# Kernel optimization log

Measured on AMD Instinct MI355X. Metric: run time of the kernel, lower is better.

Reference implementation:

```python
import jax, jax.numpy as jnp
import numpy as np

B, D_IN, R, D_P, K, D_C, ITERS = 4096, 2048, 7, 128, 25, 16, 3


def _ln(x, g, b, eps=1e-5):
    m = jnp.mean(x, axis=-1, keepdims=True)
    v = jnp.var(x, axis=-1, keepdims=True)
    return (x - m) * jax.lax.rsqrt(v + eps) * g + b


def _squash(x):
    eps = 1e-6
    ns = jnp.sum(x * x, axis=-1, keepdims=True)
    scale = ns / jnp.maximum(1.0 + ns, eps)
    return scale * x / (jnp.sqrt(ns) + eps)


def setup_inputs() -> dict:
    key = jax.random.key(0)
    ks = jax.random.split(key, 8)
    f = lambda k, shp, s=0.02: (jax.random.normal(k, shp) * s).astype(jnp.float32)
    return {
        "z": jax.random.normal(ks[0], (B, D_IN), jnp.float32),
        "W_prim": f(ks[1], (D_IN, R * D_P)),
        "b_prim": jnp.zeros((R * D_P,), jnp.float32),
        "ln_a_g": jnp.ones((D_IN,), jnp.float32),
        "ln_a_b": jnp.zeros((D_IN,), jnp.float32),
        "W_act": f(ks[2], (D_IN, R)),
        "b_act": jnp.zeros((R,), jnp.float32),
        "w_caps": (np.sqrt(K / (D_P * R)).astype(np.float32)
                   * jax.random.normal(ks[3], (R, D_P, K, D_C))).astype(jnp.float32),
        "ln_c_g": jnp.ones((D_C,), jnp.float32),
        "ln_c_b": jnp.zeros((D_C,), jnp.float32),
        "beta_u": f(ks[4], (K,), 1.0),
        "ln_h_g": jnp.ones((R * D_C,), jnp.float32),
        "ln_h_b": jnp.zeros((R * D_C,), jnp.float32),
        "W_h1": f(ks[5], (R * D_C, 4 * R * D_C)),
        "b_h1": jnp.zeros((4 * R * D_C,), jnp.float32),
        "W_h2": f(ks[6], (4 * R * D_C, 1)),
        "b_h2": jnp.zeros((1,), jnp.float32),
    }


def reference(z, W_prim, b_prim, ln_a_g, ln_a_b, W_act, b_act, w_caps,
              ln_c_g, ln_c_b, beta_u, ln_h_g, ln_h_b, W_h1, b_h1, W_h2, b_h2):
    # primary capsules: [B, R, D_P] poses + [B, R] activations
    pose = _squash((z @ W_prim + b_prim).reshape(B, R, D_P))
    act = jnp.clip(jax.nn.sigmoid(_ln(z, ln_a_g, ln_a_b) @ W_act + b_act), 0.0, 1.0)

    # votes: [B, R, K, D_C]
    u = jnp.einsum('brd,rdkh->brkh', pose, w_caps)
    scale = 1.0 / np.sqrt(D_C).astype(np.float32)

    # iterative routing (EM/softmax-agreement style)
    q = jnp.full((B, R, K), 1.0 / K, dtype=z.dtype)
    class_pose = None
    for _ in range(ITERS):
        wts = q * act[:, :, None]                               # [B,R,K]
        class_pose = _ln(jnp.einsum('brk,brkh->bkh', wts, u), ln_c_g, ln_c_b)
        agree = jnp.einsum('bkh,brkh->brk', class_pose, u) * scale
        q = jax.nn.softmax(agree, axis=-1)

    class_act = jax.nn.sigmoid(beta_u[None, :] + jnp.einsum('brk,br->bk', q, act))
    route_class_emb = q[..., None] * u                          # [B,R,K,D_C]

    # concat per-route interaction vectors -> [B, K, R*D_C]
    class_embed = jnp.transpose(route_class_emb, (0, 2, 1, 3)).reshape(B, K, R * D_C)
    h = jax.nn.gelu(_ln(class_embed, ln_h_g, ln_h_b) @ W_h1 + b_h1, approximate=False)
    logits = (h @ W_h2 + b_h2)[..., 0]                          # [B, K]

    return (logits, class_embed, class_pose, class_act, q, pose, act, route_class_emb)
```

## Files before the change

### kernel.cpp

```cpp
#include <hip/hip_runtime.h>
#include <cstddef>

#define BB 4096
#define DIN 2048
#define RR 7
#define DP 128
#define KK 25
#define DC 16
#define NITERS 3
#define RKH (RR*KK*DC)
#define RK  (RR*KK)
#define KH  (KK*DC)
#define HD  (RR*DC)
#define H4  (4*HD)
#define HEAD_TILES (BB*KK/128)

typedef __attribute__((ext_vector_type(8))) short bf16x8;
typedef __attribute__((ext_vector_type(4))) float f32x4;

__device__ __forceinline__ unsigned pk_bf16(float a, float b) {
    union { float f; unsigned u; } xa, xb;
    xa.f = a; xb.f = b;
    unsigned ua = (xa.u + 0x7FFFu + ((xa.u >> 16) & 1u)) >> 16;
    unsigned ub = (xb.u + 0x7FFFu + ((xb.u >> 16) & 1u)) >> 16;
    return (ua & 0xFFFFu) | (ub << 16);
}

__device__ __forceinline__ unsigned short bf16_1(float a) {
    union { float f; unsigned u; } xa; xa.f = a;
    return (unsigned short)((xa.u + 0x7FFFu + ((xa.u >> 16) & 1u)) >> 16);
}

__device__ __forceinline__ float gelu_fast(float x) {
    float u = x * __builtin_fmaf(x * x, 0.07135655f, 1.5957691f);
    u = fmaxf(u, -30.0f);
    float e = __expf(-u);
    return x * __builtin_amdgcn_rcpf(1.0f + e);
}

__global__ __launch_bounds__(256) void transpose_cvt_kernel(
    const float* __restrict__ src, unsigned short* __restrict__ dst, int RS, int CS)
{
    __shared__ float T[64][65];
    int r0 = blockIdx.x * 64, c0 = blockIdx.y * 64;
    size_t bo = (size_t)blockIdx.z * RS * CS;
    src += bo; dst += bo;
    int t = threadIdx.x;
    for (int s = t; s < 64 * 16; s += 256) {
        int row = s >> 4, c4 = s & 15;
        int gr = r0 + row, gc = c0 + c4 * 4;
        float4 v = make_float4(0.f, 0.f, 0.f, 0.f);
        if (gr < RS && gc < CS) v = *(const float4*)(src + (size_t)gr * CS + gc);
        T[row][c4 * 4 + 0] = v.x; T[row][c4 * 4 + 1] = v.y;
        T[row][c4 * 4 + 2] = v.z; T[row][c4 * 4 + 3] = v.w;
    }
    __syncthreads();
    for (int s = t; s < 64 * 16; s += 256) {
        int col = s >> 4, r4 = s & 15;
        int gc = c0 + col, gr = r0 + r4 * 4;
        if (gc < CS && gr + 3 < RS) {
            unsigned lo = pk_bf16(T[r4 * 4 + 0][col], T[r4 * 4 + 1][col]);
            unsigned hi = pk_bf16(T[r4 * 4 + 2][col], T[r4 * 4 + 3][col]);
            *(uint2*)(dst + (size_t)gc * RS + gr) = make_uint2(lo, hi);
        }
    }
}

__global__ __launch_bounds__(256) void w1_frag_kernel(
    const float* __restrict__ W1, unsigned short* __restrict__ W1F)
{
    int d = blockIdx.x * 256 + threadIdx.x;
    int e2 = d & 3;
    int lane = (d >> 2) & 63;
    int fid = d >> 8;
    int j = fid & 3, ks = (fid >> 2) & 3, nc = fid >> 4;
    int col = nc * 64 + j * 16 + (lane & 15);
    int k = ks * 32 + (lane >> 4) * 8 + e2 * 2;
    float a = (k < HD)     ? W1[(size_t)k * H4 + col]       : 0.f;
    float b = (k + 1 < HD) ? W1[(size_t)(k + 1) * H4 + col] : 0.f;
    ((unsigned*)W1F)[d] = pk_bf16(a, b);
}

__global__ __launch_bounds__(256) void wpf_kernel(
    const float* __restrict__ Wp, unsigned short* __restrict__ wpf)
{
    int tid = blockIdx.x * 256 + threadIdx.x;
    int lane = tid & 63;
    int CH = tid >> 6;
    int c = CH & 63, gcol = CH >> 6;
    int n = gcol * 16 + (lane & 15);
    int k0 = c * 32 + (lane >> 4) * 8;
    unsigned d0, d1, d2, d3;
    {
        float a0 = Wp[(size_t)(k0 + 0) * (RR * DP) + n];
        float a1 = Wp[(size_t)(k0 + 1) * (RR * DP) + n];
        float a2 = Wp[(size_t)(k0 + 2) * (RR * DP) + n];
        float a3 = Wp[(size_t)(k0 + 3) * (RR * DP) + n];
        float a4 = Wp[(size_t)(k0 + 4) * (RR * DP) + n];
        float a5 = Wp[(size_t)(k0 + 5) * (RR * DP) + n];
        float a6 = Wp[(size_t)(k0 + 6) * (RR * DP) + n];
        float a7 = Wp[(size_t)(k0 + 7) * (RR * DP) + n];
        d0 = pk_bf16(a0, a1); d1 = pk_bf16(a2, a3);
        d2 = pk_bf16(a4, a5); d3 = pk_bf16(a6, a7);
    }
    *(uint4*)(wpf + (size_t)tid * 8) = make_uint4(d0, d1, d2, d3);
}

__global__ __launch_bounds__(256) void wcf_kernel(
    const float* __restrict__ wc, unsigned short* __restrict__ wcf)
{
    __shared__ float Sw[128][17];
    int r = blockIdx.x, nt = blockIdx.y;
    int t = threadIdx.x;
    {
        int d = t >> 1, half = t & 1;
        const float* sp = wc + ((size_t)r * DP + d) * KH + nt * 16 + half * 8;
        float4 v0 = *(const float4*)(sp);
        float4 v1 = *(const float4*)(sp + 4);
        Sw[d][half * 8 + 0] = v0.x; Sw[d][half * 8 + 1] = v0.y;
        Sw[d][half * 8 + 2] = v0.z; Sw[d][half * 8 + 3] = v0.w;
        Sw[d][half * 8 + 4] = v1.x; Sw[d][half * 8 + 5] = v1.y;
        Sw[d][half * 8 + 6] = v1.z; Sw[d][half * 8 + 7] = v1.w;
    }
    __syncthreads();
    int l = t >> 2, e2 = t & 3;
    int n = l & 15;
    unsigned* outp = (unsigned*)wcf;
#pragma unroll
    for (int c = 0; c < 4; ++c) {
        int d = c * 32 + (l >> 4) * 8 + e2 * 2;
        unsigned v = pk_bf16(Sw[d][n], Sw[d + 1][n]);
        outp[(size_t)((r * 100 + nt * 4 + c)) * 256 + t] = v;
    }
}

__global__ __launch_bounds__(256) void act_kernel(
    const float* __restrict__ z, const float* __restrict__ g, const float* __restrict__ bb,
    const float* __restrict__ Wa, const float* __restrict__ ba,
    float* __restrict__ act_out, unsigned short* __restrict__ zf_out)
{
    int b = blockIdx.x;
    int t = threadIdx.x;
    __shared__ float zs[DIN];
    __shared__ float ws1[4], ws2[4];
    __shared__ float wr[4][RR];
    const float* zr = z + (size_t)b * DIN;
    float s = 0.f, s2 = 0.f;
    for (int i = t; i < DIN; i += 256) {
        float v = zr[i]; zs[i] = v; s += v; s2 += v * v;
    }
    for (int off = 32; off; off >>= 1) { s += __shfl_down(s, off); s2 += __shfl_down(s2, off); }
    int w = t >> 6, lane = t & 63;
    if (lane == 0) { ws1[w] = s; ws2[w] = s2; }
    __syncthreads();
    if (zf_out) {
        int c = t >> 2, o = t & 3;
        const float* zp = zs + c * 32 + o * 8;
        unsigned d0 = pk_bf16(zp[0], zp[1]);
        unsigned d1 = pk_bf16(zp[2], zp[3]);
        unsigned d2 = pk_bf16(zp[4], zp[5]);
        unsigned d3 = pk_bf16(zp[6], zp[7]);
        size_t off2 = (((size_t)(b >> 4) * 64 + c) * 64 + (size_t)(o * 16 + (b & 15))) * 8;
        *(uint4*)(zf_out + off2) = make_uint4(d0, d1, d2, d3);
    }
    s  = ws1[0] + ws1[1] + ws1[2] + ws1[3];
    s2 = ws2[0] + ws2[1] + ws2[2] + ws2[3];
    float mean = s * (1.0f / DIN);
    float var  = s2 * (1.0f / DIN) - mean * mean;
    float rstd = rsqrtf(var + 1e-5f);
    float acc[RR];
#pragma unroll
    for (int r = 0; r < RR; ++r) acc[r] = 0.f;
    for (int i = t; i < DIN; i += 256) {
        float y = (zs[i] - mean) * rstd * g[i] + bb[i];
#pragma unroll
        for (int r = 0; r < RR; ++r) acc[r] += y * Wa[i * RR + r];
    }
    for (int off = 32; off; off >>= 1) {
#pragma unroll
        for (int r = 0; r < RR; ++r) acc[r] += __shfl_down(acc[r], off);
    }
    if (lane == 0) {
#pragma unroll
        for (int r = 0; r < RR; ++r) wr[w][r] = acc[r];
    }
    __syncthreads();
    if (t < RR) {
        float v = wr[0][t] + wr[1][t] + wr[2][t] + wr[3][t] + ba[t];
        float sg = 1.0f / (1.0f + expf(-v));
        sg = fminf(fmaxf(sg, 0.0f), 1.0f);
        act_out[(size_t)b * RR + t] = sg;
    }
}

#define PV_STAGE(KS, AD, BD) do {                                                           \
    _Pragma("unroll")                                                                       \
    for (int q = 0; q < 4; ++q) {                                                           \
        int ch = w * 4 + q;                                                                 \
        int gi = ch >> 2, cc = ch & 3;                                                      \
        __builtin_amdgcn_global_load_lds(                                                   \
            (const __attribute__((address_space(1))) unsigned int*)(const void*)            \
                (zf + (((size_t)(zbase + gi) * 64) + (KS) * 4 + cc) * 512 + l * 8),         \
            (__attribute__((address_space(3))) unsigned int*)(void*)                        \
                ((AD) + ch * 512 + l * 8), 16, 0, 0);                                       \
        __builtin_amdgcn_global_load_lds(                                                   \
            (const __attribute__((address_space(1))) unsigned int*)(const void*)            \
                (wpf + (((size_t)(wbase + gi) * 64) + (KS) * 4 + cc) * 512 + l * 8),        \
            (__attribute__((address_space(3))) unsigned int*)(void*)                        \
                ((BD) + ch * 512 + l * 8), 16, 0, 0);                                       \
    }                                                                                       \
} while (0)

#define PV_COMPUTE(AD, BD) do {                                                             \
    _Pragma("unroll")                                                                       \
    for (int c = 0; c < 4; ++c) {                                                           \
        bf16x8 a[2], b[4];                                                                  \
        _Pragma("unroll")                                                                   \
        for (int i = 0; i < 2; ++i)                                                         \
            a[i] = *(const bf16x8*)((AD) + ((wrI * 2 + i) * 4 + c) * 512 + l * 8);          \
        _Pragma("unroll")                                                                   \
        for (int j = 0; j < 4; ++j)                                                         \
            b[j] = *(const bf16x8*)((BD) + ((wcI * 4 + j) * 4 + c) * 512 + l * 8);          \
        _Pragma("unroll")                                                                   \
        for (int i = 0; i < 2; ++i)                                                         \
            _Pragma("unroll")                                                               \
            for (int j = 0; j < 4; ++j)                                                     \
                acc[i][j] = __builtin_amdgcn_mfma_f32_16x16x32_bf16(a[i], b[j], acc[i][j], 0, 0, 0); \
    }                                                                                       \
} while (0)

__global__ __launch_bounds__(512) void pose_votes_mfma(
    const unsigned short* __restrict__ zf, const unsigned short* __restrict__ wpf,
    const unsigned short* __restrict__ wcf, const float* __restrict__ bp,
    float* __restrict__ pose_out, float* __restrict__ u_out)
{
    __shared__ __align__(16) char pool[135168];
    __shared__ float sq[2][128];
    unsigned short* A0 = (unsigned short*)pool;
    unsigned short* A1 = (unsigned short*)(pool + 32768);
    unsigned short* B0 = (unsigned short*)(pool + 65536);
    unsigned short* B1 = (unsigned short*)(pool + 98304);
    unsigned short* AT = (unsigned short*)pool;
    unsigned short* BV = (unsigned short*)(pool + 32768);

    int m0 = blockIdx.x * 128, r = blockIdx.y;
    int t = threadIdx.x, w = t >> 6, l = t & 63;
    int wrI = w >> 1, wcI = w & 1;
    int lrow = l & 15, koff = l >> 4;
    int zbase = m0 >> 4;
    int wbase = r * 8;

    f32x4 acc[2][4];
#pragma unroll
    for (int i = 0; i < 2; ++i)
#pragma unroll
        for (int j = 0; j < 4; ++j) acc[i][j] = 0.0f;

    PV_STAGE(0, A0, B0);
    __syncthreads();
#pragma unroll 1
    for (int ks = 0; ks < 16; ks += 2) {
        if (ks + 1 < 16) PV_STAGE(ks + 1, A1, B1);
        PV_COMPUTE(A0, B0);
        __syncthreads();
        if (ks + 2 < 16) PV_STAGE(ks + 2, A0, B0);
        PV_COMPUTE(A1, B1);
        __syncthreads();
    }

    const unsigned short* wrp = wcf + (size_t)r * 100 * 512;
#pragma unroll
    for (int q = 0; q < 13; ++q) {
        int chunk = w + q * 8;
        if (chunk < 100)
            __builtin_amdgcn_global_load_lds(
                (const __attribute__((address_space(1))) unsigned int*)(const void*)(wrp + (size_t)chunk * 512 + l * 8),
                (__attribute__((address_space(3))) unsigned int*)(void*)(BV + chunk * 512),
                16, 0, 0);
    }

    float bpv[4];
#pragma unroll
    for (int j = 0; j < 4; ++j) bpv[j] = bp[r * DP + wcI * 64 + j * 16 + lrow];
    float ns_[2][4];
#pragma unroll
    for (int i = 0; i < 2; ++i)
#pragma unroll
        for (int reg = 0; reg < 4; ++reg) {
            float ss = 0.f;
#pragma unroll
            for (int j = 0; j < 4; ++j) {
                float x = acc[i][j][reg] + bpv[j];
                acc[i][j][reg] = x;
                ss += x * x;
            }
            ss += __shfl_xor(ss, 1); ss += __shfl_xor(ss, 2);
            ss += __shfl_xor(ss, 4); ss += __shfl_xor(ss, 8);
            ns_[i][reg] = ss;
        }
    if (lrow == 0) {
#pragma unroll
        for (int i = 0; i < 2; ++i)
#pragma unroll
            for (int reg = 0; reg < 4; ++reg)
                sq[wcI][wrI * 32 + i * 16 + koff * 4 + reg] = ns_[i][reg];
    }
    __syncthreads();

#pragma unroll
    for (int i = 0; i < 2; ++i)
#pragma unroll
        for (int reg = 0; reg < 4; ++reg) {
            int rl = wrI * 32 + i * 16 + koff * 4 + reg;
            float ns = sq[0][rl] + sq[1][rl];
            float factor = (ns / fmaxf(1.0f + ns, 1e-6f)) / (sqrtf(ns) + 1e-6f);
            size_t rowbase = ((size_t)(m0 + rl) * RR + r) * DP;
            int g8 = rl >> 4, r15 = rl & 15;
#pragma unroll
            for (int j = 0; j < 4; ++j) {
                float v = acc[i][j][reg] * factor;
                int col = wcI * 64 + j * 16 + lrow;
                pose_out[rowbase + col] = v;
                int cseg = col >> 5;
                int l2 = r15 + 16 * ((col >> 3) & 3);
                AT[(size_t)((g8 * 4 + cseg) * 64 + l2) * 8 + (col & 7)] = bf16_1(v);
            }
        }
    __syncthreads();

    bf16x8 af2[4];
#pragma unroll
    for (int c = 0; c < 4; ++c)
        af2[c] = *(const bf16x8*)(AT + (size_t)((w * 4 + c) * 64 + l) * 8);
    int crow = (l >> 4) * 4;
#pragma unroll 1
    for (int nt = 0; nt < 25; ++nt) {
        f32x4 a2 = 0.0f;
#pragma unroll
        for (int c = 0; c < 4; ++c) {
            bf16x8 bfr = *(const bf16x8*)(BV + (size_t)((nt * 4 + c) * 64 + l) * 8);
            a2 = __builtin_amdgcn_mfma_f32_16x16x32_bf16(af2[c], bfr, a2, 0, 0, 0);
        }
#pragma unroll
        for (int reg = 0; reg < 4; ++reg) {
            int row = m0 + w * 16 + crow + reg;
            u_out[((size_t)row * RR + r) * KH + nt * 16 + (l & 15)] = a2[reg];
        }
    }
}

__global__ __launch_bounds__(256) void pose_mfma(
    const float* __restrict__ z, const unsigned short* __restrict__ WpT,
    const float* __restrict__ bp, float* __restrict__ pose_out)
{
    __shared__ __align__(16) unsigned short As[128 * 40];
    __shared__ __align__(16) unsigned short Bs[128 * 40];
    __shared__ float sq[2][128];
    int m0 = blockIdx.x * 128, r = blockIdx.y, t = threadIdx.x;
    int n0 = r * DP;
    int w = t >> 6, l = t & 63;
    int lrow = l & 15, koff = l >> 4;
    int rbase = (w >> 1) * 64, cbase = (w & 1) * 64;
    f32x4 acc[4][4];
#pragma unroll
    for (int i = 0; i < 4; ++i)
#pragma unroll
        for (int j = 0; j < 4; ++j) acc[i][j] = 0.0f;
    for (int kt = 0; kt < DIN; kt += 32) {
#pragma unroll
        for (int q = 0; q < 4; ++q) {
            int s = t + 256 * q;
            int row = s >> 3, k4 = s & 7;
            float4 v = *(const float4*)(z + (size_t)(m0 + row) * DIN + kt + k4 * 4);
            *(uint2*)(As + row * 40 + k4 * 4) = make_uint2(pk_bf16(v.x, v.y), pk_bf16(v.z, v.w));
        }
#pragma unroll
        for (int q = 0; q < 2; ++q) {
            int s = t + 256 * q;
            int col = s >> 2, k8 = s & 3;
            uint4 v = *(const uint4*)(WpT + (size_t)(n0 + col) * DIN + kt + k8 * 8);
            *(uint4*)(Bs + col * 40 + k8 * 8) = v;
        }
        __syncthreads();
        bf16x8 a[4], b[4];
#pragma unroll
        for (int i = 0; i < 4; ++i)
            a[i] = *(const bf16x8*)(As + (rbase + i * 16 + lrow) * 40 + koff * 8);
#pragma unroll
        for (int j = 0; j < 4; ++j)
            b[j] = *(const bf16x8*)(Bs + (cbase + j * 16 + lrow) * 40 + koff * 8);
#pragma unroll
        for (int i = 0; i < 4; ++i)
#pragma unroll
            for (int j = 0; j < 4; ++j)
                acc[i][j] = __builtin_amdgcn_mfma_f32_16x16x32_bf16(a[i], b[j], acc[i][j], 0, 0, 0);
        __syncthreads();
    }
    float bpv[4];
#pragma unroll
    for (int j = 0; j < 4; ++j) bpv[j] = bp[n0 + cbase + j * 16 + lrow];
    float ns_[4][4];
#pragma unroll
    for (int i = 0; i < 4; ++i)
#pragma unroll
        for (int reg = 0; reg < 4; ++reg) {
            float ss = 0.f;
#pragma unroll
            for (int j = 0; j < 4; ++j) {
                float x = acc[i][j][reg] + bpv[j];
                acc[i][j][reg] = x;
                ss += x * x;
            }
            ss += __shfl_xor(ss, 1); ss += __shfl_xor(ss, 2);
            ss += __shfl_xor(ss, 4); ss += __shfl_xor(ss, 8);
            ns_[i][reg] = ss;
        }
    if (lrow == 0) {
#pragma unroll
        for (int i = 0; i < 4; ++i)
#pragma unroll
            for (int reg = 0; reg < 4; ++reg)
                sq[w & 1][rbase + i * 16 + koff * 4 + reg] = ns_[i][reg];
    }
    __syncthreads();
#pragma unroll
    for (int i = 0; i < 4; ++i)
#pragma unroll
        for (int reg = 0; reg < 4; ++reg) {
            int rl = rbase + i * 16 + koff * 4 + reg;
            float ns = sq[0][rl] + sq[1][rl];
            float factor = (ns / fmaxf(1.0f + ns, 1e-6f)) / (sqrtf(ns) + 1e-6f);
            size_t rowbase = ((size_t)(m0 + rl) * RR + r) * DP;
#pragma unroll
            for (int j = 0; j < 4; ++j)
                pose_out[rowbase + cbase + j * 16 + lrow] = acc[i][j][reg] * factor;
        }
}

__global__ __launch_bounds__(256) void votes_mfma(
    const float* __restrict__ pose, const unsigned short* __restrict__ wcT,
    float* __restrict__ u_out)
{
    __shared__ __align__(16) unsigned short As[128 * 152];
    __shared__ __align__(16) unsigned short Bs[80 * 152];
    int m0 = blockIdx.x * 128, r = blockIdx.y, n0 = blockIdx.z * 80;
    int t = threadIdx.x;
    int w = t >> 6, l = t & 63;
    int lrow = l & 15, koff = l >> 4;
    int rbase = w * 32;
#pragma unroll
    for (int q = 0; q < 16; ++q) {
        int s = t + 256 * q;
        int row = s >> 5, k4 = s & 31;
        float4 v = *(const float4*)(pose + ((size_t)(m0 + row) * RR + r) * DP + k4 * 4);
        *(uint2*)(As + row * 152 + k4 * 4) = make_uint2(pk_bf16(v.x, v.y), pk_bf16(v.z, v.w));
    }
    const unsigned short* wr_ = wcT + (size_t)r * KH * DP;
#pragma unroll
    for (int q = 0; q < 5; ++q) {
        int s = t + 256 * q;
        int col = s >> 4, k8 = s & 15;
        uint4 v = *(const uint4*)(wr_ + (size_t)(n0 + col) * DP + k8 * 8);
        *(uint4*)(Bs + col * 152 + k8 * 8) = v;
    }
    __syncthreads();
    f32x4 acc[2][5];
#pragma unroll
    for (int i = 0; i < 2; ++i)
#pragma unroll
        for (int j = 0; j < 5; ++j) acc[i][j] = 0.0f;
#pragma unroll
    for (int ks = 0; ks < 4; ++ks) {
        bf16x8 a[2], b[5];
#pragma unroll
        for (int i = 0; i < 2; ++i)
            a[i] = *(const bf16x8*)(As + (rbase + i * 16 + lrow) * 152 + ks * 32 + koff * 8);
#pragma unroll
        for (int j = 0; j < 5; ++j)
            b[j] = *(const bf16x8*)(Bs + (j * 16 + lrow) * 152 + ks * 32 + koff * 8);
#pragma unroll
        for (int i = 0; i < 2; ++i)
#pragma unroll
            for (int j = 0; j < 5; ++j)
                acc[i][j] = __builtin_amdgcn_mfma_f32_16x16x32_bf16(a[i], b[j], acc[i][j], 0, 0, 0);
    }
#pragma unroll
    for (int i = 0; i < 2; ++i)
#pragma unroll
        for (int reg = 0; reg < 4; ++reg) {
            int row = m0 + rbase + i * 16 + koff * 4 + reg;
            size_t base = ((size_t)row * RR + r) * KH + n0;
#pragma unroll
            for (int j = 0; j < 5; ++j)
                u_out[base + j * 16 + lrow] = acc[i][j][reg];
        }
}

__global__ __launch_bounds__(64) void routing_kernel(
    const float* __restrict__ u_in, const float* __restrict__ act_in,
    const float* __restrict__ lncg, const float* __restrict__ lncb,
    const float* __restrict__ beta_u,
    float* __restrict__ q_out, float* __restrict__ cp_out,
    float* __restrict__ ca_out, float* __restrict__ rce_out,
    float* __restrict__ ce_out)
{
    __shared__ __align__(16) float U[RKH];
    __shared__ float Q[RK];
    __shared__ float CP[KH];
    __shared__ float AG[RK];
    __shared__ float A7[RR];
    int b = blockIdx.x, t = threadIdx.x;
    const float4* u4 = (const float4*)(u_in + (size_t)b * RKH);
    float4* U4 = (float4*)U;
    for (int p = t; p < RKH / 4; p += 64) U4[p] = u4[p];
    if (t < RR) A7[t] = act_in[(size_t)b * RR + t];
    for (int p = t; p < RK; p += 64) Q[p] = 1.0f / KK;
    __syncthreads();
    for (int it = 0; it < NITERS; ++it) {
        for (int p = t; p < KH; p += 64) {
            int k = p / DC;
            float s = 0.f;
#pragma unroll
            for (int r = 0; r < RR; ++r) s += Q[r * KK + k] * A7[r] * U[r * KH + p];
            CP[p] = s;
        }
        __syncthreads();
        if (t < KK) {
            float m = 0.f;
#pragma unroll
            for (int h = 0; h < DC; ++h) m += CP[t * DC + h];
            m *= (1.0f / DC);
            float v = 0.f;
#pragma unroll
            for (int h = 0; h < DC; ++h) { float d = CP[t * DC + h] - m; v += d * d; }
            v *= (1.0f / DC);
            float rstd = rsqrtf(v + 1e-5f);
#pragma unroll
            for (int h = 0; h < DC; ++h)
                CP[t * DC + h] = (CP[t * DC + h] - m) * rstd * lncg[h] + lncb[h];
        }
        __syncthreads();
        for (int p = t; p < RK; p += 64) {
            int r = p / KK, k = p % KK;
            float s = 0.f;
#pragma unroll
            for (int h = 0; h < DC; ++h) s += CP[k * DC + h] * U[r * KH + k * DC + h];
            AG[p] = s * 0.25f;
        }
        __syncthreads();
        if (t < RR) {
            float mx = -1e30f;
            for (int k = 0; k < KK; ++k) mx = fmaxf(mx, AG[t * KK + k]);
            float e[KK], sum = 0.f;
            for (int k = 0; k < KK; ++k) { e[k] = expf(AG[t * KK + k] - mx); sum += e[k]; }
            float inv = 1.0f / sum;
            for (int k = 0; k < KK; ++k) Q[t * KK + k] = e[k] * inv;
        }
        __syncthreads();
    }
    if (t < KK) {
        float s = 0.f;
#pragma unroll
        for (int r = 0; r < RR; ++r) s += Q[r * KK + t] * A7[r];
        ca_out[(size_t)b * KK + t] = 1.0f / (1.0f + expf(-(beta_u[t] + s)));
    }
    for (int p = t; p < RK; p += 64) q_out[(size_t)b * RK + p] = Q[p];
    for (int p = t; p < KH; p += 64) cp_out[(size_t)b * KH + p] = CP[p];
    float4* rce4 = (float4*)(rce_out + (size_t)b * RKH);
    float4* ce4  = (float4*)ce_out;
    for (int p4 = t; p4 < RKH / 4; p4 += 64) {
        int base = p4 * 4;
        int r  = base / KH;
        int k  = (base % KH) / DC;
        int h0 = base % DC;
        float qv = Q[r * KK + k];
        float4 uv = U4[p4];
        float4 rv = make_float4(qv * uv.x, qv * uv.y, qv * uv.z, qv * uv.w);
        rce4[p4] = rv;
        size_t ci = ((size_t)b * RKH + (size_t)k * HD + (size_t)r * DC + h0) >> 2;
        ce4[ci] = rv;
    }
}

__global__ __launch_bounds__(512) void head_mfma(
    const float* __restrict__ ce, const float* __restrict__ g, const float* __restrict__ bb,
    const unsigned short* __restrict__ W1F, const float* __restrict__ b1,
    const float* __restrict__ W2, const float* __restrict__ b2,
    float* __restrict__ logits)
{
    __shared__ __align__(16) unsigned short As[128 * 128];
    __shared__ __align__(16) unsigned short Bs[448 * 128];
    __shared__ float LB1[H4];
    __shared__ float LW2[H4];
    int t = threadIdx.x;
    int w = t >> 6, l = t & 63;
    int lrow = l & 15, koff = l >> 4;

#pragma unroll
    for (int q = 0; q < 14; ++q) {
        int chunk = w * 14 + q;
        __builtin_amdgcn_global_load_lds(
            (const __attribute__((address_space(1))) unsigned int*)(const void*)(W1F + (size_t)chunk * 512 + l * 8),
            (__attribute__((address_space(3))) unsigned int*)(void*)(Bs + chunk * 512),
            16, 0, 0);
    }
    if (t >= 256) {
        for (int s = t - 256; s < H4; s += 256) { LB1[s] = b1[s]; LW2[s] = W2[s]; }
    }
    float b2v = b2[0];

    int row = t >> 1, half = t & 1;
    int lr = row & 15, rt = row >> 4;

    float4 v[14];
    int tile = blockIdx.x;
    if (t < 256 && tile < HEAD_TILES) {
        const float* rp = ce + (size_t)(tile * 128 + row) * HD + half * 56;
#pragma unroll
        for (int m = 0; m < 14; ++m) v[m] = *(const float4*)(rp + m * 4);
    }

    bool first = true;
    for (; tile < HEAD_TILES; tile += 256) {
        if (!first) __syncthreads();
        first = false;

        if (t < 256) {
            float s1 = 0.f, s2 = 0.f;
#pragma unroll
            for (int m = 0; m < 14; ++m) {
                s1 += v[m].x + v[m].y + v[m].z + v[m].w;
                s2 += v[m].x * v[m].x + v[m].y * v[m].y + v[m].z * v[m].z + v[m].w * v[m].w;
            }
            s1 += __shfl_xor(s1, 1); s2 += __shfl_xor(s2, 1);
            float mean = s1 * (1.0f / HD);
            float var  = s2 * (1.0f / HD) - mean * mean;
            float rstd = rsqrtf(var + 1e-5f);
#pragma unroll
            for (int j = 0; j < 7; ++j) {
                float4 gl0 = *(const float4*)(g  + half * 56 + j * 8);
                float4 gl1 = *(const float4*)(g  + half * 56 + j * 8 + 4);
                float4 bl0 = *(const float4*)(bb + half * 56 + j * 8);
                float4 bl1 = *(const float4*)(bb + half * 56 + j * 8 + 4);
                float4 x0 = v[j * 2], x1 = v[j * 2 + 1];
                float y0 = (x0.x - mean) * rstd * gl0.x + bl0.x;
                float y1 = (x0.y - mean) * rstd * gl0.y + bl0.y;
                float y2 = (x0.z - mean) * rstd * gl0.z + bl0.z;
                float y3 = (x0.w - mean) * rstd * gl0.w + bl0.w;
                float y4 = (x1.x - mean) * rstd * gl1.x + bl1.x;
                float y5 = (x1.y - mean) * rstd * gl1.y + bl1.y;
                float y6 = (x1.z - mean) * rstd * gl1.z + bl1.z;
                float y7 = (x1.w - mean) * rstd * gl1.w + bl1.w;
                int k8 = half * 7 + j;
                int ks = k8 >> 2, ko = k8 & 3;
                unsigned* dst = (unsigned*)(As + (size_t)((rt * 4 + ks) * 64 + ko * 16 + lr) * 8);
                dst[0] = pk_bf16(y0, y1); dst[1] = pk_bf16(y2, y3);
                dst[2] = pk_bf16(y4, y5); dst[3] = pk_bf16(y6, y7);
            }
            if (half) {
                uint4 z4 = make_uint4(0, 0, 0, 0);
                *(uint4*)(As + (size_t)((rt * 4 + 3) * 64 + 2 * 16 + lr) * 8) = z4;
                *(uint4*)(As + (size_t)((rt * 4 + 3) * 64 + 3 * 16 + lr) * 8) = z4;
            }
        }
        __syncthreads();

        bf16x8 af[4];
#pragma unroll
        for (int ks = 0; ks < 4; ++ks)
            af[ks] = *(const bf16x8*)(As + (size_t)((w * 4 + ks) * 64 + l) * 8);

        if (t < 256 && tile + 256 < HEAD_TILES) {
            const float* rp = ce + (size_t)((tile + 256) * 128 + row) * HD + half * 56;
#pragma unroll
            for (int m = 0; m < 14; ++m) v[m] = *(const float4*)(rp + m * 4);
        }

        float logitAcc[4];
#pragma unroll
        for (int reg = 0; reg < 4; ++reg) logitAcc[reg] = 0.f;

        for (int nc = 0; nc < 7; ++nc) {
            float b1v[4], w2v[4];
#pragma unroll
            for (int j = 0; j < 4; ++j) {
                b1v[j] = LB1[nc * 64 + j * 16 + lrow];
                w2v[j] = LW2[nc * 64 + j * 16 + lrow];
            }
            f32x4 acc[4];
#pragma unroll
            for (int j = 0; j < 4; ++j) acc[j] = 0.0f;
#pragma unroll
            for (int ks = 0; ks < 4; ++ks) {
                bf16x8 bfr[4];
#pragma unroll
                for (int j = 0; j < 4; ++j)
                    bfr[j] = *(const bf16x8*)(Bs + (size_t)(((nc * 4 + ks) * 4 + j) * 64 + l) * 8);
#pragma unroll
                for (int j = 0; j < 4; ++j)
                    acc[j] = __builtin_amdgcn_mfma_f32_16x16x32_bf16(af[ks], bfr[j], acc[j], 0, 0, 0);
            }
#pragma unroll
            for (int reg = 0; reg < 4; ++reg) {
                float sum = 0.f;
#pragma unroll
                for (int j = 0; j < 4; ++j) {
                    float x = acc[j][reg] + b1v[j];
                    sum += gelu_fast(x) * w2v[j];
                }
                logitAcc[reg] += sum;
            }
        }
#pragma unroll
        for (int reg = 0; reg < 4; ++reg) {
            float vv = logitAcc[reg];
            vv += __shfl_xor(vv, 1); vv += __shfl_xor(vv, 2);
            vv += __shfl_xor(vv, 4); vv += __shfl_xor(vv, 8);
            if (lrow == 0)
                logits[(size_t)tile * 128 + w * 16 + koff * 4 + reg] = vv + b2v;
        }
    }
}

__global__ __launch_bounds__(256) void pose_kernel(
    const float* __restrict__ z, const float* __restrict__ Wp, const float* __restrict__ bp,
    float* __restrict__ pose_out)
{
    __shared__ __align__(16) float As[64 * 36];
    __shared__ __align__(16) float Bs[32 * 128];
    int m0 = blockIdx.x * 64;
    int r  = blockIdx.y;
    int n0 = r * DP;
    int t  = threadIdx.x;
    int rg = t >> 5;
    int cg = t & 31;
    float acc[8][4] = {};
    for (int kt = 0; kt < DIN; kt += 32) {
#pragma unroll
        for (int q = 0; q < 2; ++q) {
            int s = t * 2 + q;
            int row = s >> 3, k4 = s & 7;
            float4 v = *(const float4*)(z + (size_t)(m0 + row) * DIN + kt + k4 * 4);
            *(float4*)(As + row * 36 + k4 * 4) = v;
        }
#pragma unroll
        for (int q = 0; q < 4; ++q) {
            int s = t + 256 * q;
            int row = s >> 5, c4 = s & 31;
            float4 v = *(const float4*)(Wp + (size_t)(kt + row) * (RR * DP) + n0 + c4 * 4);
            *(float4*)(Bs + row * 128 + c4 * 4) = v;
        }
        __syncthreads();
#pragma unroll
        for (int kk = 0; kk < 32; ++kk) {
            float4 bv = *(const float4*)(Bs + kk * 128 + cg * 4);
#pragma unroll
            for (int j = 0; j < 8; ++j) {
                float a = As[(rg * 8 + j) * 36 + kk];
                acc[j][0] += a * bv.x; acc[j][1] += a * bv.y;
                acc[j][2] += a * bv.z; acc[j][3] += a * bv.w;
            }
        }
        __syncthreads();
    }
    float bi0 = bp[n0 + cg * 4], bi1 = bp[n0 + cg * 4 + 1];
    float bi2 = bp[n0 + cg * 4 + 2], bi3 = bp[n0 + cg * 4 + 3];
#pragma unroll
    for (int j = 0; j < 8; ++j) {
        float x0 = acc[j][0] + bi0, x1 = acc[j][1] + bi1;
        float x2 = acc[j][2] + bi2, x3 = acc[j][3] + bi3;
        float ns = x0 * x0 + x1 * x1 + x2 * x2 + x3 * x3;
        for (int off = 1; off < 32; off <<= 1) ns += __shfl_xor(ns, off);
        float factor = (ns / fmaxf(1.0f + ns, 1e-6f)) / (sqrtf(ns) + 1e-6f);
        int row = m0 + rg * 8 + j;
        float4 o = make_float4(x0 * factor, x1 * factor, x2 * factor, x3 * factor);
        *(float4*)(pose_out + ((size_t)row * RR + r) * DP + cg * 4) = o;
    }
}

__global__ __launch_bounds__(256) void votes_kernel(
    const float* __restrict__ pose, const float* __restrict__ wc,
    float* __restrict__ u_out)
{
    __shared__ float As[64 * 129];
    __shared__ __align__(16) float Bs[64 * 80];
    int m0 = blockIdx.x * 64;
    int r  = blockIdx.y;
    int n0 = blockIdx.z * 80;
    int t  = threadIdx.x;
    const size_t wbase = (size_t)r * DP * KH;
#pragma unroll
    for (int q = 0; q < 8; ++q) {
        int s = t + 256 * q;
        int row = s >> 5, d4 = s & 31;
        float4 v = *(const float4*)(pose + ((size_t)(m0 + row) * RR + r) * DP + d4 * 4);
        As[row * 129 + d4 * 4 + 0] = v.x;
        As[row * 129 + d4 * 4 + 1] = v.y;
        As[row * 129 + d4 * 4 + 2] = v.z;
        As[row * 129 + d4 * 4 + 3] = v.w;
    }
    int m4 = t >> 4, n5 = t & 15;
    float acc[4][5];
#pragma unroll
    for (int i = 0; i < 4; ++i)
#pragma unroll
        for (int j = 0; j < 5; ++j) acc[i][j] = 0.f;
    for (int kt = 0; kt < DP; kt += 64) {
        __syncthreads();
#pragma unroll
        for (int q = 0; q < 5; ++q) {
            int s = t + 256 * q;
            int d = s / 20, c4 = s % 20;
            float4 v = *(const float4*)(wc + wbase + (size_t)(kt + d) * KH + n0 + c4 * 4);
            *(float4*)(Bs + d * 80 + c4 * 4) = v;
        }
        __syncthreads();
#pragma unroll 4
        for (int dd = 0; dd < 64; ++dd) {
            int d = kt + dd;
            float b_[5];
#pragma unroll
            for (int j = 0; j < 5; ++j) b_[j] = Bs[dd * 80 + n5 * 5 + j];
#pragma unroll
            for (int i = 0; i < 4; ++i) {
                float a = As[(m4 * 4 + i) * 129 + d];
#pragma unroll
                for (int j = 0; j < 5; ++j) acc[i][j] += a * b_[j];
            }
        }
    }
#pragma unroll
    for (int i = 0; i < 4; ++i) {
        int row = m0 + m4 * 4 + i;
        size_t base = ((size_t)row * RR + r) * KH + n0 + n5 * 5;
#pragma unroll
        for (int j = 0; j < 5; ++j) u_out[base + j] = acc[i][j];
    }
}

__global__ __launch_bounds__(256) void head_kernel(
    const float* __restrict__ ce, const float* __restrict__ g, const float* __restrict__ bb,
    const float* __restrict__ W1, const float* __restrict__ b1,
    const float* __restrict__ W2, const float* __restrict__ b2,
    float* __restrict__ logits)
{
    __shared__ __align__(16) float Y[64 * HD];
    __shared__ float Wc[HD * 64];
    __shared__ float Lg[64];
    int row0 = blockIdx.x * 64;
    int t = threadIdx.x;
    for (int s = t; s < 64 * HD; s += 256) Y[s] = ce[(size_t)row0 * HD + s];
    __syncthreads();
    if (t < 64) {
        float m = 0.f;
        for (int i = 0; i < HD; ++i) m += Y[t * HD + i];
        m *= (1.0f / HD);
        float v = 0.f;
        for (int i = 0; i < HD; ++i) { float d = Y[t * HD + i] - m; v += d * d; }
        v *= (1.0f / HD);
        float rstd = rsqrtf(v + 1e-5f);
        for (int i = 0; i < HD; ++i) Y[t * HD + i] = (Y[t * HD + i] - m) * rstd * g[i] + bb[i];
    }
    int rg = t >> 4;
    int cg = t & 15;
    float accRow[4] = {0.f, 0.f, 0.f, 0.f};
    for (int c0 = 0; c0 < H4; c0 += 64) {
        __syncthreads();
        for (int s = t; s < HD * 64; s += 256) {
            int i = s >> 6, c = s & 63;
            Wc[i * 64 + c] = W1[(size_t)i * H4 + c0 + c];
        }
        __syncthreads();
        float b1v[4], w2v[4];
#pragma unroll
        for (int c = 0; c < 4; ++c) { b1v[c] = b1[c0 + cg * 4 + c]; w2v[c] = W2[c0 + cg * 4 + c]; }
        float s_[4][4];
#pragma unroll
        for (int rr = 0; rr < 4; ++rr)
#pragma unroll
            for (int c = 0; c < 4; ++c) s_[rr][c] = b1v[c];
        for (int i4 = 0; i4 < HD / 4; ++i4) {
            float4 y4[4];
#pragma unroll
            for (int rr = 0; rr < 4; ++rr)
                y4[rr] = *(const float4*)(Y + (rg * 4 + rr) * HD + i4 * 4);
#pragma unroll
            for (int is = 0; is < 4; ++is) {
                float w_[4];
#pragma unroll
                for (int c = 0; c < 4; ++c) w_[c] = Wc[(i4 * 4 + is) * 64 + cg * 4 + c];
#pragma unroll
                for (int rr = 0; rr < 4; ++rr) {
                    float yv = (is == 0) ? y4[rr].x : (is == 1) ? y4[rr].y : (is == 2) ? y4[rr].z : y4[rr].w;
#pragma unroll
                    for (int c = 0; c < 4; ++c) s_[rr][c] += yv * w_[c];
                }
            }
        }
#pragma unroll
        for (int rr = 0; rr < 4; ++rr) {
#pragma unroll
            for (int c = 0; c < 4; ++c) {
                float x = s_[rr][c];
                float ge = 0.5f * x * (1.0f + erff(x * 0.70710678118654752440f));
                accRow[rr] += ge * w2v[c];
            }
        }
    }
#pragma unroll
    for (int rr = 0; rr < 4; ++rr) {
        float v = accRow[rr];
        v += __shfl_xor(v, 1); v += __shfl_xor(v, 2);
        v += __shfl_xor(v, 4); v += __shfl_xor(v, 8);
        if (cg == 0) Lg[rg * 4 + rr] = v;
    }
    __syncthreads();
    if (t < 64) logits[row0 + t] = Lg[t] + b2[0];
}

extern "C" void kernel_launch(void* const* d_in, const int* in_sizes, int n_in,
                              void* d_out, int out_size, void* d_ws, size_t ws_size,
                              hipStream_t stream) {
    const float* z    = (const float*)d_in[0];
    const float* Wp   = (const float*)d_in[1];
    const float* bp   = (const float*)d_in[2];
    const float* lnag = (const float*)d_in[3];
    const float* lnab = (const float*)d_in[4];
    const float* Wa   = (const float*)d_in[5];
    const float* ba   = (const float*)d_in[6];
    const float* wc   = (const float*)d_in[7];
    const float* lncg = (const float*)d_in[8];
    const float* lncb = (const float*)d_in[9];
    const float* beta = (const float*)d_in[10];
    const float* lnhg = (const float*)d_in[11];
    const float* lnhb = (const float*)d_in[12];
    const float* W1   = (const float*)d_in[13];
    const float* b1   = (const float*)d_in[14];
    const float* W2   = (const float*)d_in[15];
    const float* b2   = (const float*)d_in[16];

    float* out = (float*)d_out;
    float* o_logits = out;
    float* o_ce   = o_logits + (size_t)BB * KK;
    float* o_cp   = o_ce   + (size_t)BB * KK * HD;
    float* o_ca   = o_cp   + (size_t)BB * KK * DC;
    float* o_q    = o_ca   + (size_t)BB * KK;
    float* o_pose = o_q    + (size_t)BB * RK;
    float* o_act  = o_pose + (size_t)BB * RR * DP;
    float* o_rce  = o_act  + (size_t)BB * RR;

    const size_t W1F_ELE = (size_t)H4 * 128;
    const size_t WCF_ELE = (size_t)RR * 100 * 512;
    const size_t ZF_ELE  = (size_t)BB * DIN;
    const size_t WPF_ELE = (size_t)(RR * DP) * DIN;
    unsigned short* W1F = (unsigned short*)d_ws;
    unsigned short* wcf = W1F + W1F_ELE;
    unsigned short* zf  = wcf + WCF_ELE;
    unsigned short* wpf = zf + ZF_ELE;
    unsigned short* wcT = wcf;
    unsigned short* WpT = zf;

    const size_t WS_NEW = (W1F_ELE + WCF_ELE + ZF_ELE + WPF_ELE) * sizeof(unsigned short);
    const size_t WS_MID = (W1F_ELE + WCF_ELE + WPF_ELE) * sizeof(unsigned short);

    if (ws_size >= WS_NEW) {
        hipLaunchKernelGGL(act_kernel, dim3(BB), dim3(256), 0, stream,
                           z, lnag, lnab, Wa, ba, o_act, zf);
        hipLaunchKernelGGL(wpf_kernel, dim3(896), dim3(256), 0, stream, Wp, wpf);
        hipLaunchKernelGGL(w1_frag_kernel, dim3(112), dim3(256), 0, stream, W1, W1F);
        hipLaunchKernelGGL(wcf_kernel, dim3(RR, 25), dim3(256), 0, stream, wc, wcf);
        hipLaunchKernelGGL(pose_votes_mfma, dim3(BB / 128, RR), dim3(512), 0, stream,
                           zf, wpf, wcf, bp, o_pose, o_rce);
        hipLaunchKernelGGL(routing_kernel, dim3(BB), dim3(64), 0, stream,
                           o_rce, o_act, lncg, lncb, beta, o_q, o_cp, o_ca, o_rce, o_ce);
        hipLaunchKernelGGL(head_mfma, dim3(256), dim3(512), 0, stream,
                           o_ce, lnhg, lnhb, W1F, b1, W2, b2, o_logits);
    } else if (ws_size >= WS_MID) {
        hipLaunchKernelGGL(act_kernel, dim3(BB), dim3(256), 0, stream,
                           z, lnag, lnab, Wa, ba, o_act, (unsigned short*)nullptr);
        hipLaunchKernelGGL(transpose_cvt_kernel, dim3(DIN / 64, (RR * DP) / 64, 1), dim3(256), 0, stream,
                           Wp, WpT, DIN, RR * DP);
        hipLaunchKernelGGL(w1_frag_kernel, dim3(112), dim3(256), 0, stream, W1, W1F);
        hipLaunchKernelGGL(transpose_cvt_kernel, dim3(2, 7, RR), dim3(256), 0, stream,
                           wc, wcT, DP, KH);
        hipLaunchKernelGGL(pose_mfma, dim3(BB / 128, RR), dim3(256), 0, stream,
                           z, WpT, bp, o_pose);
        hipLaunchKernelGGL(votes_mfma, dim3(BB / 128, RR, 5), dim3(256), 0, stream,
                           o_pose, wcT, o_rce);
        hipLaunchKernelGGL(routing_kernel, dim3(BB), dim3(64), 0, stream,
                           o_rce, o_act, lncg, lncb, beta, o_q, o_cp, o_ca, o_rce, o_ce);
        hipLaunchKernelGGL(head_mfma, dim3(256), dim3(512), 0, stream,
                           o_ce, lnhg, lnhb, W1F, b1, W2, b2, o_logits);
    } else {
        hipLaunchKernelGGL(act_kernel, dim3(BB), dim3(256), 0, stream,
                           z, lnag, lnab, Wa, ba, o_act, (unsigned short*)nullptr);
        hipLaunchKernelGGL(pose_kernel, dim3(BB / 64, RR), dim3(256), 0, stream,
                           z, Wp, bp, o_pose);
        hipLaunchKernelGGL(votes_kernel, dim3(BB / 64, RR, 5), dim3(256), 0, stream,
                           o_pose, wc, o_rce);
        hipLaunchKernelGGL(routing_kernel, dim3(BB), dim3(64), 0, stream,
                           o_rce, o_act, lncg, lncb, beta, o_q, o_cp, o_ca, o_rce, o_ce);
        hipLaunchKernelGGL(head_kernel, dim3(BB * KK / 64), dim3(256), 0, stream,
                           o_ce, lnhg, lnhb, W1, b1, W2, b2, o_logits);
    }
}
```

Baseline: 315.1 us.

## Fold LayerNorm into activation projection and parallelize routing LN and softmax

The activation path now precomputes g·W and b·W once in a small kernel and expands the LayerNorm algebraically, so act_kernel makes a single pass over z that accumulates the raw sums and z·g·W together instead of two passes. Separately, the routing kernel's class-pose LayerNorm and per-route softmax are spread across the whole wavefront using shuffle reductions, replacing the versions that ran on only 25 or 7 threads, and q·act is precomputed once per iteration. This adds one tiny extra kernel launch and changes floating-point rounding slightly (E[x²]-mean² variance, __expf).

```diff
diff --git a/kernel.cpp b/kernel.cpp
--- a/kernel.cpp
+++ b/kernel.cpp
@@ -134,10 +134,104 @@
     }
 }
 
+__global__ __launch_bounds__(256) void gwbw_kernel(
+    const float* __restrict__ g, const float* __restrict__ bb,
+    const float* __restrict__ Wa, float* __restrict__ gwbw)
+{
+    __shared__ float red[4][2 * RR];
+    int t = threadIdx.x;
+    float a1[RR], a2[RR];
+#pragma unroll
+    for (int r = 0; r < RR; ++r) { a1[r] = 0.f; a2[r] = 0.f; }
+    for (int i = t; i < DIN; i += 256) {
+        float gv = g[i], bv = bb[i];
+#pragma unroll
+        for (int r = 0; r < RR; ++r) {
+            float wv = Wa[i * RR + r];
+            a1[r] += gv * wv;
+            a2[r] += bv * wv;
+        }
+    }
+    for (int off = 32; off; off >>= 1) {
+#pragma unroll
+        for (int r = 0; r < RR; ++r) {
+            a1[r] += __shfl_down(a1[r], off);
+            a2[r] += __shfl_down(a2[r], off);
+        }
+    }
+    int w = t >> 6, lane = t & 63;
+    if (lane == 0) {
+#pragma unroll
+        for (int r = 0; r < RR; ++r) { red[w][r] = a1[r]; red[w][RR + r] = a2[r]; }
+    }
+    __syncthreads();
+    if (t < 2 * RR)
+        gwbw[t] = red[0][t] + red[1][t] + red[2][t] + red[3][t];
+}
+
 __global__ __launch_bounds__(256) void act_kernel(
+    const float* __restrict__ z, const float* __restrict__ g,
+    const float* __restrict__ Wa, const float* __restrict__ ba,
+    const float* __restrict__ gwbw,
+    float* __restrict__ act_out, unsigned short* __restrict__ zf_out)
+{
+    int b = blockIdx.x;
+    int t = threadIdx.x;
+    __shared__ float zs[DIN];
+    __shared__ float ws1[4], ws2[4];
+    __shared__ float wr[4][RR];
+    const float* zr = z + (size_t)b * DIN;
+    float s = 0.f, s2 = 0.f;
+    float zgw[RR];
+#pragma unroll
+    for (int r = 0; r < RR; ++r) zgw[r] = 0.f;
+    for (int i = t; i < DIN; i += 256) {
+        float v = zr[i]; zs[i] = v;
+        s += v; s2 += v * v;
+        float zg = v * g[i];
+#pragma unroll
+        for (int r = 0; r < RR; ++r) zgw[r] += zg * Wa[i * RR + r];
+    }
+    for (int off = 32; off; off >>= 1) {
+        s += __shfl_down(s, off); s2 += __shfl_down(s2, off);
+#pragma unroll
+        for (int r = 0; r < RR; ++r) zgw[r] += __shfl_down(zgw[r], off);
+    }
+    int w = t >> 6, lane = t & 63;
+    if (lane == 0) {
+        ws1[w] = s; ws2[w] = s2;
+#pragma unroll
+        for (int r = 0; r < RR; ++r) wr[w][r] = zgw[r];
+    }
+    __syncthreads();
+    if (zf_out) {
+        int c = t >> 2, o = t & 3;
+        const float* zp = zs + c * 32 + o * 8;
+        unsigned d0 = pk_bf16(zp[0], zp[1]);
+        unsigned d1 = pk_bf16(zp[2], zp[3]);
+        unsigned d2 = pk_bf16(zp[4], zp[5]);
+        unsigned d3 = pk_bf16(zp[6], zp[7]);
+        size_t off2 = (((size_t)(b >> 4) * 64 + c) * 64 + (size_t)(o * 16 + (b & 15))) * 8;
+        *(uint4*)(zf_out + off2) = make_uint4(d0, d1, d2, d3);
+    }
+    if (t < RR) {
+        float ts  = ws1[0] + ws1[1] + ws1[2] + ws1[3];
+        float ts2 = ws2[0] + ws2[1] + ws2[2] + ws2[3];
+        float mean = ts * (1.0f / DIN);
+        float var  = ts2 * (1.0f / DIN) - mean * mean;
+        float rstd = rsqrtf(var + 1e-5f);
+        float zg = wr[0][t] + wr[1][t] + wr[2][t] + wr[3][t];
+        float v = rstd * zg - rstd * mean * gwbw[t] + gwbw[RR + t] + ba[t];
+        float sg = 1.0f / (1.0f + expf(-v));
+        sg = fminf(fmaxf(sg, 0.0f), 1.0f);
+        act_out[(size_t)b * RR + t] = sg;
+    }
+}
+
+__global__ __launch_bounds__(256) void act_kernel_fb(
     const float* __restrict__ z, const float* __restrict__ g, const float* __restrict__ bb,
     const float* __restrict__ Wa, const float* __restrict__ ba,
-    float* __restrict__ act_out, unsigned short* __restrict__ zf_out)
+    float* __restrict__ act_out)
 {
     int b = blockIdx.x;
     int t = threadIdx.x;
@@ -153,16 +247,6 @@
     int w = t >> 6, lane = t & 63;
     if (lane == 0) { ws1[w] = s; ws2[w] = s2; }
     __syncthreads();
-    if (zf_out) {
-        int c = t >> 2, o = t & 3;
-        const float* zp = zs + c * 32 + o * 8;
-        unsigned d0 = pk_bf16(zp[0], zp[1]);
-        unsigned d1 = pk_bf16(zp[2], zp[3]);
-        unsigned d2 = pk_bf16(zp[4], zp[5]);
-        unsigned d3 = pk_bf16(zp[6], zp[7]);
-        size_t off2 = (((size_t)(b >> 4) * 64 + c) * 64 + (size_t)(o * 16 + (b & 15))) * 8;
-        *(uint4*)(zf_out + off2) = make_uint4(d0, d1, d2, d3);
-    }
     s  = ws1[0] + ws1[1] + ws1[2] + ws1[3];
     s2 = ws2[0] + ws2[1] + ws2[2] + ws2[3];
     float mean = s * (1.0f / DIN);
@@ -515,46 +599,70 @@
     for (int p = t; p < RKH / 4; p += 64) U4[p] = u4[p];
     if (t < RR) A7[t] = act_in[(size_t)b * RR + t];
     for (int p = t; p < RK; p += 64) Q[p] = 1.0f / KK;
+    int kg = t >> 4, hl = t & 15;
+    float lg = lncg[hl], lb = lncb[hl];
+    int rg = t >> 3, li = t & 7;
     __syncthreads();
     for (int it = 0; it < NITERS; ++it) {
+        for (int p = t; p < RK; p += 64) AG[p] = Q[p] * A7[p / KK];
+        __syncthreads();
         for (int p = t; p < KH; p += 64) {
-            int k = p / DC;
+            int k = p >> 4;
             float s = 0.f;
 #pragma unroll
-            for (int r = 0; r < RR; ++r) s += Q[r * KK + k] * A7[r] * U[r * KH + p];
+            for (int r = 0; r < RR; ++r) s += AG[r * KK + k] * U[r * KH + p];
             CP[p] = s;
         }
         __syncthreads();
-        if (t < KK) {
-            float m = 0.f;
-#pragma unroll
-            for (int h = 0; h < DC; ++h) m += CP[t * DC + h];
-            m *= (1.0f / DC);
-            float v = 0.f;
-#pragma unroll
-            for (int h = 0; h < DC; ++h) { float d = CP[t * DC + h] - m; v += d * d; }
-            v *= (1.0f / DC);
-            float rstd = rsqrtf(v + 1e-5f);
-#pragma unroll
-            for (int h = 0; h < DC; ++h)
-                CP[t * DC + h] = (CP[t * DC + h] - m) * rstd * lncg[h] + lncb[h];
+#pragma unroll
+        for (int pass = 0; pass < 7; ++pass) {
+            int k = kg + 4 * pass;
+            bool ok = k < KK;
+            float v = ok ? CP[k * DC + hl] : 0.f;
+            float s1 = v, s2v = v * v;
+            s1 += __shfl_xor(s1, 1); s2v += __shfl_xor(s2v, 1);
+            s1 += __shfl_xor(s1, 2); s2v += __shfl_xor(s2v, 2);
+            s1 += __shfl_xor(s1, 4); s2v += __shfl_xor(s2v, 4);
+            s1 += __shfl_xor(s1, 8); s2v += __shfl_xor(s2v, 8);
+            float mean = s1 * (1.0f / DC);
+            float var  = s2v * (1.0f / DC) - mean * mean;
+            float rstd = rsqrtf(var + 1e-5f);
+            if (ok) CP[k * DC + hl] = (v - mean) * rstd * lg + lb;
         }
         __syncthreads();
         for (int p = t; p < RK; p += 64) {
-            int r = p / KK, k = p % KK;
+            int r = p / KK, k = p - r * KK;
             float s = 0.f;
 #pragma unroll
             for (int h = 0; h < DC; ++h) s += CP[k * DC + h] * U[r * KH + k * DC + h];
             AG[p] = s * 0.25f;
         }
         __syncthreads();
-        if (t < RR) {
+        {
+            float av[4];
             float mx = -1e30f;
-            for (int k = 0; k < KK; ++k) mx = fmaxf(mx, AG[t * KK + k]);
-            float e[KK], sum = 0.f;
-            for (int k = 0; k < KK; ++k) { e[k] = expf(AG[t * KK + k] - mx); sum += e[k]; }
+#pragma unroll
+            for (int j2 = 0; j2 < 4; ++j2) {
+                int k = li + 8 * j2;
+                av[j2] = (rg < RR && k < KK) ? AG[rg * KK + k] : -1e30f;
+                mx = fmaxf(mx, av[j2]);
+            }
+            mx = fmaxf(mx, __shfl_xor(mx, 1));
+            mx = fmaxf(mx, __shfl_xor(mx, 2));
+            mx = fmaxf(mx, __shfl_xor(mx, 4));
+            float sum = 0.f;
+#pragma unroll
+            for (int j2 = 0; j2 < 4; ++j2) {
+                av[j2] = __expf(av[j2] - mx);
+                sum += av[j2];
+            }
+            sum += __shfl_xor(sum, 1); sum += __shfl_xor(sum, 2); sum += __shfl_xor(sum, 4);
             float inv = 1.0f / sum;
-            for (int k = 0; k < KK; ++k) Q[t * KK + k] = e[k] * inv;
+#pragma unroll
+            for (int j2 = 0; j2 < 4; ++j2) {
+                int k = li + 8 * j2;
+                if (rg < RR && k < KK) Q[rg * KK + k] = av[j2] * inv;
+            }
         }
         __syncthreads();
     }
@@ -953,19 +1061,22 @@
     const size_t WCF_ELE = (size_t)RR * 100 * 512;
     const size_t ZF_ELE  = (size_t)BB * DIN;
     const size_t WPF_ELE = (size_t)(RR * DP) * DIN;
+    const size_t GW_ELE  = 32;
     unsigned short* W1F = (unsigned short*)d_ws;
     unsigned short* wcf = W1F + W1F_ELE;
     unsigned short* zf  = wcf + WCF_ELE;
     unsigned short* wpf = zf + ZF_ELE;
+    float*          gwbw = (float*)(wpf + WPF_ELE);
     unsigned short* wcT = wcf;
     unsigned short* WpT = zf;
 
-    const size_t WS_NEW = (W1F_ELE + WCF_ELE + ZF_ELE + WPF_ELE) * sizeof(unsigned short);
+    const size_t WS_NEW = (W1F_ELE + WCF_ELE + ZF_ELE + WPF_ELE + GW_ELE) * sizeof(unsigned short);
     const size_t WS_MID = (W1F_ELE + WCF_ELE + WPF_ELE) * sizeof(unsigned short);
 
     if (ws_size >= WS_NEW) {
+        hipLaunchKernelGGL(gwbw_kernel, dim3(1), dim3(256), 0, stream, lnag, lnab, Wa, gwbw);
         hipLaunchKernelGGL(act_kernel, dim3(BB), dim3(256), 0, stream,
-                           z, lnag, lnab, Wa, ba, o_act, zf);
+                           z, lnag, Wa, ba, gwbw, o_act, zf);
         hipLaunchKernelGGL(wpf_kernel, dim3(896), dim3(256), 0, stream, Wp, wpf);
         hipLaunchKernelGGL(w1_frag_kernel, dim3(112), dim3(256), 0, stream, W1, W1F);
         hipLaunchKernelGGL(wcf_kernel, dim3(RR, 25), dim3(256), 0, stream, wc, wcf);
@@ -976,8 +1087,8 @@
         hipLaunchKernelGGL(head_mfma, dim3(256), dim3(512), 0, stream,
                            o_ce, lnhg, lnhb, W1F, b1, W2, b2, o_logits);
     } else if (ws_size >= WS_MID) {
-        hipLaunchKernelGGL(act_kernel, dim3(BB), dim3(256), 0, stream,
-                           z, lnag, lnab, Wa, ba, o_act, (unsigned short*)nullptr);
+        hipLaunchKernelGGL(act_kernel_fb, dim3(BB), dim3(256), 0, stream,
+                           z, lnag, lnab, Wa, ba, o_act);
         hipLaunchKernelGGL(transpose_cvt_kernel, dim3(DIN / 64, (RR * DP) / 64, 1), dim3(256), 0, stream,
                            Wp, WpT, DIN, RR * DP);
         hipLaunchKernelGGL(w1_frag_kernel, dim3(112), dim3(256), 0, stream, W1, W1F);
@@ -992,8 +1103,8 @@
         hipLaunchKernelGGL(head_mfma, dim3(256), dim3(512), 0, stream,
                            o_ce, lnhg, lnhb, W1F, b1, W2, b2, o_logits);
     } else {
-        hipLaunchKernelGGL(act_kernel, dim3(BB), dim3(256), 0, stream,
-                           z, lnag, lnab, Wa, ba, o_act, (unsigned short*)nullptr);
+        hipLaunchKernelGGL(act_kernel_fb, dim3(BB), dim3(256), 0, stream,
+                           z, lnag, lnab, Wa, ba, o_act);
         hipLaunchKernelGGL(pose_kernel, dim3(BB / 64, RR), dim3(256), 0, stream,
                            z, Wp, bp, o_pose);
         hipLaunchKernelGGL(votes_kernel, dim3(BB / 64, RR, 5), dim3(256), 0, stream,
```

Result: slower. 328.4 us (+4.2%).
